# Performance work log

Hardware: AMD Instinct MI355X
Metric: run time of the kernel (lower is better)

The kernel has to match this reference:

```python
import jax, jax.numpy as jnp
import numpy as np

NUM_HEADS = 4

def setup_inputs() -> dict:
    key = jax.random.key(0)
    ks = jax.random.split(key, 8)
    B, L, D, Lc = 4, 4096, 256, 4096
    s = 0.02
    return {
        "x": jax.random.normal(ks[0], (B, L, D), jnp.float32),
        "context": jax.random.normal(ks[1], (B, Lc, D), jnp.float32),
        "Wq": jax.random.normal(ks[2], (D, D), jnp.float32) * s,
        "bq": jax.random.normal(ks[3], (D,), jnp.float32) * s,
        "Wkv": jax.random.normal(ks[4], (D, 2 * D), jnp.float32) * s,
        "bkv": jax.random.normal(ks[5], (2 * D,), jnp.float32) * s,
        "Wp": jax.random.normal(ks[6], (D, D), jnp.float32) * s,
        "bp": jax.random.normal(ks[7], (D,), jnp.float32) * s,
    }


def reference(x, context, Wq, bq, Wkv, bkv, Wp, bp):
    B, L, D = x.shape
    Hn = NUM_HEADS
    hd = D // Hn
    Hs = Ws = int(L ** 0.5)
    scale = hd ** (-0.5)

    # projections
    q = (x @ Wq + bq).reshape(B, L, Hn, hd).transpose(0, 2, 1, 3)        # [B,H,L,hd]
    kv = (context @ Wkv + bkv).reshape(B, -1, 2, Hn, hd)
    k = kv[:, :, 0].transpose(0, 2, 1, 3)                                 # [B,H,Lc,hd]
    v = kv[:, :, 1].transpose(0, 2, 1, 3)                                 # [B,H,Lc,hd]

    attn = jnp.einsum('bhqd,bhkd->bhqk', q, k) * scale                    # [B,H,L,Lc]
    attn_weights = jax.nn.softmax(attn, axis=-1)

    attn_map = attn_weights.mean(axis=1).sum(axis=-1).reshape(B, Hs, Ws)  # [B,H,W]

    out = jnp.einsum('bhqk,bhkd->bhqd', attn_weights, v)                  # [B,H,L,hd]
    out = out.transpose(0, 2, 1, 3).reshape(B, L, D)
    out = out @ Wp + bp
    return (out + x, attn_map)
```

## Files before the change

kernel.cpp:

```cpp
#include <hip/hip_runtime.h>
#include <stdint.h>

typedef unsigned short u16;
typedef short s16x8 __attribute__((ext_vector_type(8)));
typedef u16   u16x8 __attribute__((ext_vector_type(8)));
typedef float f32x4 __attribute__((ext_vector_type(4)));
typedef float f32x16 __attribute__((ext_vector_type(16)));

#define QSCALE 0.180336880111169f

__device__ __forceinline__ u16 f2bf(float f) {
  union { float f; uint32_t u; } v; v.f = f;
  uint32_t r = (v.u + 0x7fffu + ((v.u >> 16) & 1u)) >> 16;
  return (u16)r;
}

__device__ __forceinline__ f32x4 mfma16(s16x8 a, s16x8 b, f32x4 c) {
  return __builtin_amdgcn_mfma_f32_16x16x32_bf16(a, b, c, 0, 0, 0);
}
__device__ __forceinline__ f32x16 mfma32(s16x8 a, s16x8 b, f32x16 c) {
  return __builtin_amdgcn_mfma_f32_32x32x16_bf16(a, b, c, 0, 0, 0);
}

__device__ __forceinline__ void gload16(const void* g, void* l) {
  __builtin_amdgcn_global_load_lds(
      (const __attribute__((address_space(1))) void*)g,
      (__attribute__((address_space(3))) void*)l, 16, 0, 0);
}

__device__ __forceinline__ s16x8 ldsr(const u16* base, int row, int colb) {
  return *(const s16x8*)((const char*)base + row * 128 + (colb ^ ((row & 7) << 4)));
}

__device__ __forceinline__ uint32_t cvtpk(float lo, float hi) {
  uint32_t r;
  asm("v_cvt_pk_bf16_f32 %0, %1, %2" : "=v"(r) : "v"(lo), "v"(hi));
  return r;
}
__device__ __forceinline__ void hswap(uint32_t& a, uint32_t& b) {
  asm("v_permlane32_swap_b32 %0, %1" : "+v"(a), "+v"(b));
}
__device__ __forceinline__ float cross_sum(float v) {
  float t = v, u = v;
  asm("v_permlane32_swap_b32 %0, %1" : "+v"(t), "+v"(u));
  return t + u;
}

__global__ void k_convert(const float* __restrict__ x, const float* __restrict__ ctx,
                          const float* __restrict__ wq, const float* __restrict__ wkv,
                          const float* __restrict__ wp,
                          u16* __restrict__ xb, u16* __restrict__ cb,
                          u16* __restrict__ wqT, u16* __restrict__ wkvT,
                          u16* __restrict__ wpT, float* __restrict__ amap) {
  int tid = blockIdx.x * 256 + threadIdx.x;
  if (tid < 2097152) {
    const float* src; u16* dst; int off;
    if (tid < 1048576) { src = x;   dst = xb; off = tid * 4; }
    else               { src = ctx; dst = cb; off = (tid - 1048576) * 4; }
    f32x4 v = *(const f32x4*)(src + off);
    u16* d = dst + off;
    d[0] = f2bf(v.x); d[1] = f2bf(v.y); d[2] = f2bf(v.z); d[3] = f2bf(v.w);
    if (tid < 16384) amap[tid] = 1.0f;
  } else {
    int t4 = (tid - 2097152) * 4;
#pragma unroll
    for (int j = 0; j < 4; j++) {
      int t = t4 + j;
      if (t < 65536) {
        int k = t >> 8, n = t & 255;
        wqT[n * 256 + k] = f2bf(wq[t]);
      } else if (t < 196608) {
        int t2 = t - 65536;
        int k = t2 >> 9, n = t2 & 511;
        wkvT[n * 256 + k] = f2bf(wkv[t2]);
      } else {
        int t2 = t - 196608;
        int k = t2 >> 8, n = t2 & 255;
        wpT[n * 256 + k] = f2bf(wp[t2]);
      }
    }
  }
}

template<int EPI>
__global__ __launch_bounds__(256, 2) void k_gemm(
    const u16* __restrict__ A, const u16* __restrict__ Bt,
    const float* __restrict__ bias, const float* __restrict__ xres,
    u16* __restrict__ o16a, u16* __restrict__ o16b, float* __restrict__ o32) {
  __shared__ u16 Als[2][128 * 64];
  __shared__ u16 Bls[2][64 * 64];
  const int m0 = blockIdx.x * 128;
  const int n0 = blockIdx.y * 64;
  const int tid = threadIdx.x, w = tid >> 6, l = tid & 63;
  const int lr = l & 15, lg = l >> 4;
  const int wm = (w >> 1) * 64, wn = (w & 1) * 32;

  auto stage = [&](int buf, int k0) {
    const char* sa = (const char*)A;
#pragma unroll
    for (int i = 0; i < 4; i++) {
      int dbase = (w * 4 + i) * 1024;
      int d = dbase + l * 16;
      int row = d >> 7, colb = d & 127;
      gload16(sa + (size_t)(m0 + row) * 512 + k0 * 2 + (colb ^ ((row & 7) << 4)),
              (char*)Als[buf] + dbase);
    }
    const char* sb = (const char*)Bt;
#pragma unroll
    for (int i = 0; i < 2; i++) {
      int dbase = (w * 2 + i) * 1024;
      int d = dbase + l * 16;
      int row = d >> 7, colb = d & 127;
      gload16(sb + (size_t)(n0 + row) * 512 + k0 * 2 + (colb ^ ((row & 7) << 4)),
              (char*)Bls[buf] + dbase);
    }
  };

  f32x4 acc[4][2];
#pragma unroll
  for (int i = 0; i < 4; i++)
#pragma unroll
    for (int j = 0; j < 2; j++) acc[i][j] = (f32x4){0.f, 0.f, 0.f, 0.f};

  stage(0, 0);
  __syncthreads();
  int cur = 0;
  for (int ks = 0; ks < 4; ks++) {
    if (ks < 3) stage(cur ^ 1, (ks + 1) * 64);
    s16x8 a[4][2], b[2][2];
#pragma unroll
    for (int mt = 0; mt < 4; mt++)
#pragma unroll
      for (int kf = 0; kf < 2; kf++)
        a[mt][kf] = ldsr(Als[cur], wm + mt * 16 + lr, lg * 16 + kf * 64);
#pragma unroll
    for (int nt = 0; nt < 2; nt++)
#pragma unroll
      for (int kf = 0; kf < 2; kf++)
        b[nt][kf] = ldsr(Bls[cur], wn + nt * 16 + lr, lg * 16 + kf * 64);
#pragma unroll
    for (int mt = 0; mt < 4; mt++)
#pragma unroll
      for (int nt = 0; nt < 2; nt++) {
        acc[mt][nt] = mfma16(a[mt][0], b[nt][0], acc[mt][nt]);
        acc[mt][nt] = mfma16(a[mt][1], b[nt][1], acc[mt][nt]);
      }
    __syncthreads();
    cur ^= 1;
  }

#pragma unroll
  for (int mt = 0; mt < 4; mt++)
#pragma unroll
    for (int nt = 0; nt < 2; nt++)
#pragma unroll
      for (int r = 0; r < 4; r++) {
        int gm = m0 + wm + mt * 16 + lg * 4 + r;
        int gn = n0 + wn + nt * 16 + lr;
        float val = acc[mt][nt][r] + bias[gn];
        if constexpr (EPI == 0) {
          int b_ = gm >> 12, ql = gm & 4095, h = gn >> 6, dd = gn & 63;
          o16a[(((size_t)(b_ * 4 + h) * 4096 + ql) << 6) + dd] = f2bf(val * QSCALE);
        } else if constexpr (EPI == 1) {
          int b_ = gm >> 12, ql = gm & 4095;
          int s = gn >> 8, inner = gn & 255, h = inner >> 6, dd = inner & 63;
          if (s) {
            size_t addr = (((size_t)(b_ * 4 + h) * 64 + (ql >> 6)) * 64 + dd) * 64 + (ql & 63);
            o16b[addr] = f2bf(val);
          } else {
            size_t addr = (((size_t)(b_ * 4 + h) * 4096 + ql) << 6) + dd;
            o16a[addr] = f2bf(val);
          }
        } else {
          size_t idx = (size_t)gm * 256 + gn;
          o32[idx] = val + xres[idx];
        }
      }
}

__global__ __launch_bounds__(256, 2) void k_flash(
    const u16* __restrict__ qb, const u16* __restrict__ kb,
    const u16* __restrict__ vtb, u16* __restrict__ ob) {
  __shared__ u16 kls[3][4096];
  __shared__ u16 vls[3][4096];
  __shared__ float lsum_lds[4][32];
  const int id = blockIdx.y * 32 + blockIdx.x;
  const int sw = (id & 7) * 64 + (id >> 3);
  const int bh = sw >> 5;
  const int q0 = (sw & 31) * 128;
  const int tid = threadIdx.x, w = tid >> 6, l = tid & 63;
  const int lr32 = l & 31, hi = l >> 5;
  const char* kbase  = (const char*)(kb + (size_t)bh * 262144);
  const char* vtbase = (const char*)(vtb + (size_t)bh * 262144);

  s16x8 qf[4];
  {
    const u16* qp = qb + ((size_t)bh * 4096 + q0 + w * 32 + lr32) * 64 + hi * 8;
#pragma unroll
    for (int mm = 0; mm < 4; mm++) qf[mm] = *(const s16x8*)(qp + mm * 16);
  }

  auto stage = [&](int buf, int t) {
    const char* ks = kbase  + (size_t)t * 8192;
    const char* vs = vtbase + (size_t)t * 8192;
#pragma unroll
    for (int i = 0; i < 2; i++) {
      int dbase = (w * 2 + i) * 1024;
      int d = dbase + l * 16;
      int row = d >> 7, colb = d & 127;
      int so = row * 128 + (colb ^ ((row & 7) << 4));
      gload16(ks + so, (char*)kls[buf] + dbase);
      gload16(vs + so, (char*)vls[buf] + dbase);
    }
  };

  f32x16 o0, o1;
  float lsum = 0.f;
#pragma unroll
  for (int r = 0; r < 16; r++) { o0[r] = 0.f; o1[r] = 0.f; }

  auto pv = [&](const f32x16& p, const u16* vc, int bcol0) {
#pragma unroll
    for (int ks2 = 0; ks2 < 2; ks2++) {
      uint32_t A0 = cvtpk(p[8 * ks2 + 0], p[8 * ks2 + 1]);
      uint32_t A1 = cvtpk(p[8 * ks2 + 2], p[8 * ks2 + 3]);
      uint32_t B0 = cvtpk(p[8 * ks2 + 4], p[8 * ks2 + 5]);
      uint32_t B1 = cvtpk(p[8 * ks2 + 6], p[8 * ks2 + 7]);
      hswap(A0, B0);
      hswap(A1, B1);
      union { uint32_t wv[4]; s16x8 h; } pa;
      pa.wv[0] = A0; pa.wv[1] = A1; pa.wv[2] = B0; pa.wv[3] = B1;
      s16x8 v0 = ldsr(vc, lr32,      bcol0 + 32 * ks2 + 16 * hi);
      s16x8 v1 = ldsr(vc, 32 + lr32, bcol0 + 32 * ks2 + 16 * hi);
      __builtin_amdgcn_s_setprio(1);
      o0 = mfma32(pa.h, v0, o0);
      o1 = mfma32(pa.h, v1, o1);
      __builtin_amdgcn_s_setprio(0);
    }
  };

  stage(0, 0);
  stage(1, 1);
  for (int t = 0; t < 64; t++) {
    if (t < 63) asm volatile("s_waitcnt vmcnt(4)" ::: "memory");
    else        asm volatile("s_waitcnt vmcnt(0)" ::: "memory");
    __builtin_amdgcn_s_barrier();
    asm volatile("" ::: "memory");
    if (t < 62) stage((t + 2) % 3, t + 2);
    const u16* kc = kls[t % 3];
    const u16* vc = vls[t % 3];

    f32x16 s0, s1;
#pragma unroll
    for (int r = 0; r < 16; r++) { s0[r] = 0.f; s1[r] = 0.f; }
    __builtin_amdgcn_s_setprio(1);
#pragma unroll
    for (int mm = 0; mm < 4; mm++) {
      s16x8 kf0 = ldsr(kc, lr32,      mm * 32 + 16 * hi);
      s16x8 kf1 = ldsr(kc, 32 + lr32, mm * 32 + 16 * hi);
      s0 = mfma32(kf0, qf[mm], s0);
      s1 = mfma32(kf1, qf[mm], s1);
    }
    __builtin_amdgcn_s_setprio(0);
#pragma unroll
    for (int r = 0; r < 16; r++) {
      s0[r] = __builtin_amdgcn_exp2f(s0[r]);
      s1[r] = __builtin_amdgcn_exp2f(s1[r]);
    }
    float acc = 0.f;
#pragma unroll
    for (int r = 0; r < 16; r++) acc += s0[r] + s1[r];
    lsum += acc;
    pv(s0, vc, 0);
    pv(s1, vc, 64);
  }

  float ltot = cross_sum(lsum);
  lsum_lds[w][lr32] = ltot;
  const int b_ = bh >> 2, h = bh & 3;
  u16* obase = ob + (size_t)b_ * 4096 * 256 + h * 64;
#pragma unroll
  for (int r = 0; r < 16; r++) {
    int crow = (r & 3) + 8 * (r >> 2) + 4 * hi;
    float inv = __builtin_amdgcn_rcpf(lsum_lds[w][crow]);
    size_t qrow = (size_t)(q0 + w * 32 + crow);
    obase[qrow * 256 + lr32]      = f2bf(o0[r] * inv);
    obase[qrow * 256 + 32 + lr32] = f2bf(o1[r] * inv);
  }
}

extern "C" void kernel_launch(void* const* d_in, const int* in_sizes, int n_in,
                              void* d_out, int out_size, void* d_ws, size_t ws_size,
                              hipStream_t stream) {
  const float* x   = (const float*)d_in[0];
  const float* ctx = (const float*)d_in[1];
  const float* Wq  = (const float*)d_in[2];
  const float* bq  = (const float*)d_in[3];
  const float* Wkv = (const float*)d_in[4];
  const float* bkv = (const float*)d_in[5];
  const float* Wp  = (const float*)d_in[6];
  const float* bp  = (const float*)d_in[7];

  char* ws = (char*)d_ws;
  u16* xb    = (u16*)(ws);
  u16* cb    = (u16*)(ws + 8388608);
  u16* wqT   = (u16*)(ws + 16777216);
  u16* wkvT  = (u16*)(ws + 16908288);
  u16* wpT   = (u16*)(ws + 17170432);
  u16* qbuf  = (u16*)(ws + 17301504);
  u16* kbuf  = (u16*)(ws + 25690112);
  u16* vtbuf = (u16*)(ws + 34078720);
  u16* aout  = (u16*)(ws + 42467328);
  float* out  = (float*)d_out;
  float* amap = out + 4194304;

  k_convert<<<8448, 256, 0, stream>>>(x, ctx, Wq, Wkv, Wp, xb, cb, wqT, wkvT, wpT, amap);
  k_gemm<0><<<dim3(128, 4), 256, 0, stream>>>(xb, wqT, bq, nullptr, qbuf, nullptr, nullptr);
  k_gemm<1><<<dim3(128, 8), 256, 0, stream>>>(cb, wkvT, bkv, nullptr, kbuf, vtbuf, nullptr);
  k_flash<<<dim3(32, 16), 256, 0, stream>>>(qbuf, kbuf, vtbuf, aout);
  k_gemm<2><<<dim3(128, 4), 256, 0, stream>>>(aout, wpT, bp, x, nullptr, nullptr, out);
}
```

Measured before the change: 133.9 us.

## Split KV range across warp pairs in flash kernel with 64-row query tiles

The flash-attention kernel now handles 64 query rows per block instead of 128 and launches twice as many blocks. Within a block, two warps share each 32-row query slice and each takes one half of every 64-key tile. The two partial outputs and row sums are then combined through LDS. The K/V staging moves from a triple buffer to a double buffer with a full vmcnt(0) wait, and launch bounds rise to 4 blocks per CU. The goal is more parallelism and occupancy, at the cost of less prefetch depth, twice the total K/V global reads, and an extra reduction step.

```diff
diff --git a/kernel.cpp b/kernel.cpp
--- a/kernel.cpp
+++ b/kernel.cpp
@@ -178,40 +178,46 @@
       }
 }
 
-__global__ __launch_bounds__(256, 2) void k_flash(
+__global__ __launch_bounds__(256, 4) void k_flash(
     const u16* __restrict__ qb, const u16* __restrict__ kb,
     const u16* __restrict__ vtb, u16* __restrict__ ob) {
-  __shared__ u16 kls[3][4096];
-  __shared__ u16 vls[3][4096];
-  __shared__ float lsum_lds[4][32];
+  __shared__ char smem[33024];
+  u16* kls0 = (u16*)(smem);
+  u16* kls1 = (u16*)(smem + 8192);
+  u16* vls0 = (u16*)(smem + 16384);
+  u16* vls1 = (u16*)(smem + 24576);
+  float* comb = (float*)smem;
+  float* lsb  = (float*)(smem + 32768);
   const int id = blockIdx.y * 32 + blockIdx.x;
-  const int sw = (id & 7) * 64 + (id >> 3);
-  const int bh = sw >> 5;
-  const int q0 = (sw & 31) * 128;
+  const int sw = (id & 7) * 128 + (id >> 3);
+  const int bh = sw >> 6;
+  const int q0 = (sw & 63) * 64;
   const int tid = threadIdx.x, w = tid >> 6, l = tid & 63;
   const int lr32 = l & 31, hi = l >> 5;
+  const int qh = w & 1, kvh = w >> 1;
   const char* kbase  = (const char*)(kb + (size_t)bh * 262144);
   const char* vtbase = (const char*)(vtb + (size_t)bh * 262144);
 
   s16x8 qf[4];
   {
-    const u16* qp = qb + ((size_t)bh * 4096 + q0 + w * 32 + lr32) * 64 + hi * 8;
+    const u16* qp = qb + ((size_t)bh * 4096 + q0 + qh * 32 + lr32) * 64 + hi * 8;
 #pragma unroll
     for (int mm = 0; mm < 4; mm++) qf[mm] = *(const s16x8*)(qp + mm * 16);
   }
 
-  auto stage = [&](int buf, int t) {
+  auto stage = [&](u16* kbuf, u16* vbuf, int t) {
     const char* ks = kbase  + (size_t)t * 8192;
     const char* vs = vtbase + (size_t)t * 8192;
+    int dbase = w * 2048 + (l >> 6) * 1024;
 #pragma unroll
     for (int i = 0; i < 2; i++) {
-      int dbase = (w * 2 + i) * 1024;
-      int d = dbase + l * 16;
+      int d = w * 2048 + i * 1024 + l * 16;
       int row = d >> 7, colb = d & 127;
       int so = row * 128 + (colb ^ ((row & 7) << 4));
-      gload16(ks + so, (char*)kls[buf] + dbase);
-      gload16(vs + so, (char*)vls[buf] + dbase);
-    }
+      gload16(ks + so, (char*)kbuf + d);
+      gload16(vs + so, (char*)vbuf + d);
+    }
+    (void)dbase;
   };
 
   f32x16 o0, o1;
@@ -219,19 +225,37 @@
 #pragma unroll
   for (int r = 0; r < 16; r++) { o0[r] = 0.f; o1[r] = 0.f; }
 
-  auto pv = [&](const f32x16& p, const u16* vc, int bcol0) {
+  auto compute = [&](const u16* kc, const u16* vc) {
+    s16x8 kf[4];
+#pragma unroll
+    for (int mm = 0; mm < 4; mm++)
+      kf[mm] = ldsr(kc, kvh * 32 + lr32, mm * 32 + 16 * hi);
+    f32x16 s;
+#pragma unroll
+    for (int r = 0; r < 16; r++) s[r] = 0.f;
+    __builtin_amdgcn_s_setprio(1);
+#pragma unroll
+    for (int mm = 0; mm < 4; mm++) s = mfma32(kf[mm], qf[mm], s);
+    __builtin_amdgcn_s_setprio(0);
+#pragma unroll
+    for (int r = 0; r < 16; r++) s[r] = __builtin_amdgcn_exp2f(s[r]);
+    float acc = 0.f;
+#pragma unroll
+    for (int r = 0; r < 16; r++) acc += s[r];
+    lsum += acc;
 #pragma unroll
     for (int ks2 = 0; ks2 < 2; ks2++) {
-      uint32_t A0 = cvtpk(p[8 * ks2 + 0], p[8 * ks2 + 1]);
-      uint32_t A1 = cvtpk(p[8 * ks2 + 2], p[8 * ks2 + 3]);
-      uint32_t B0 = cvtpk(p[8 * ks2 + 4], p[8 * ks2 + 5]);
-      uint32_t B1 = cvtpk(p[8 * ks2 + 6], p[8 * ks2 + 7]);
+      uint32_t A0 = cvtpk(s[8 * ks2 + 0], s[8 * ks2 + 1]);
+      uint32_t A1 = cvtpk(s[8 * ks2 + 2], s[8 * ks2 + 3]);
+      uint32_t B0 = cvtpk(s[8 * ks2 + 4], s[8 * ks2 + 5]);
+      uint32_t B1 = cvtpk(s[8 * ks2 + 6], s[8 * ks2 + 7]);
       hswap(A0, B0);
       hswap(A1, B1);
       union { uint32_t wv[4]; s16x8 h; } pa;
       pa.wv[0] = A0; pa.wv[1] = A1; pa.wv[2] = B0; pa.wv[3] = B1;
-      s16x8 v0 = ldsr(vc, lr32,      bcol0 + 32 * ks2 + 16 * hi);
-      s16x8 v1 = ldsr(vc, 32 + lr32, bcol0 + 32 * ks2 + 16 * hi);
+      int vcol = kvh * 64 + 32 * ks2 + 16 * hi;
+      s16x8 v0 = ldsr(vc, lr32,      vcol);
+      s16x8 v1 = ldsr(vc, 32 + lr32, vcol);
       __builtin_amdgcn_s_setprio(1);
       o0 = mfma32(pa.h, v0, o0);
       o1 = mfma32(pa.h, v1, o1);
@@ -239,53 +263,47 @@
     }
   };
 
-  stage(0, 0);
-  stage(1, 1);
-  for (int t = 0; t < 64; t++) {
-    if (t < 63) asm volatile("s_waitcnt vmcnt(4)" ::: "memory");
-    else        asm volatile("s_waitcnt vmcnt(0)" ::: "memory");
+  stage(kls0, vls0, 0);
+#pragma unroll 1
+  for (int tt = 0; tt < 32; tt++) {
+    const int t = tt * 2;
+    asm volatile("s_waitcnt vmcnt(0)" ::: "memory");
     __builtin_amdgcn_s_barrier();
     asm volatile("" ::: "memory");
-    if (t < 62) stage((t + 2) % 3, t + 2);
-    const u16* kc = kls[t % 3];
-    const u16* vc = vls[t % 3];
-
-    f32x16 s0, s1;
-#pragma unroll
-    for (int r = 0; r < 16; r++) { s0[r] = 0.f; s1[r] = 0.f; }
-    __builtin_amdgcn_s_setprio(1);
-#pragma unroll
-    for (int mm = 0; mm < 4; mm++) {
-      s16x8 kf0 = ldsr(kc, lr32,      mm * 32 + 16 * hi);
-      s16x8 kf1 = ldsr(kc, 32 + lr32, mm * 32 + 16 * hi);
-      s0 = mfma32(kf0, qf[mm], s0);
-      s1 = mfma32(kf1, qf[mm], s1);
-    }
-    __builtin_amdgcn_s_setprio(0);
+    stage(kls1, vls1, t + 1);
+    compute(kls0, vls0);
+    asm volatile("s_waitcnt vmcnt(0)" ::: "memory");
+    __builtin_amdgcn_s_barrier();
+    asm volatile("" ::: "memory");
+    if (t + 2 < 64) stage(kls0, vls0, t + 2);
+    compute(kls1, vls1);
+  }
+
+  float ltot = cross_sum(lsum);
+  __syncthreads();
+  if (kvh == 1) {
+    float* cp = comb + ((size_t)qh * 64 + l) * 33;
+#pragma unroll
+    for (int r = 0; r < 16; r++) { cp[r] = o0[r]; cp[16 + r] = o1[r]; }
+    cp[32] = ltot;
+  }
+  __syncthreads();
+  if (kvh == 0) {
+    const float* cp = comb + ((size_t)qh * 64 + l) * 33;
+#pragma unroll
+    for (int r = 0; r < 16; r++) { o0[r] += cp[r]; o1[r] += cp[16 + r]; }
+    ltot += cp[32];
+    lsb[qh * 32 + lr32] = ltot;
+    const int b_ = bh >> 2, h = bh & 3;
+    u16* obase = ob + (size_t)b_ * 4096 * 256 + h * 64;
 #pragma unroll
     for (int r = 0; r < 16; r++) {
-      s0[r] = __builtin_amdgcn_exp2f(s0[r]);
-      s1[r] = __builtin_amdgcn_exp2f(s1[r]);
-    }
-    float acc = 0.f;
-#pragma unroll
-    for (int r = 0; r < 16; r++) acc += s0[r] + s1[r];
-    lsum += acc;
-    pv(s0, vc, 0);
-    pv(s1, vc, 64);
-  }
-
-  float ltot = cross_sum(lsum);
-  lsum_lds[w][lr32] = ltot;
-  const int b_ = bh >> 2, h = bh & 3;
-  u16* obase = ob + (size_t)b_ * 4096 * 256 + h * 64;
-#pragma unroll
-  for (int r = 0; r < 16; r++) {
-    int crow = (r & 3) + 8 * (r >> 2) + 4 * hi;
-    float inv = __builtin_amdgcn_rcpf(lsum_lds[w][crow]);
-    size_t qrow = (size_t)(q0 + w * 32 + crow);
-    obase[qrow * 256 + lr32]      = f2bf(o0[r] * inv);
-    obase[qrow * 256 + 32 + lr32] = f2bf(o1[r] * inv);
+      int crow = (r & 3) + 8 * (r >> 2) + 4 * hi;
+      float inv = __builtin_amdgcn_rcpf(lsb[qh * 32 + crow]);
+      size_t qrow = (size_t)(q0 + qh * 32 + crow);
+      obase[qrow * 256 + lr32]      = f2bf(o0[r] * inv);
+      obase[qrow * 256 + 32 + lr32] = f2bf(o1[r] * inv);
+    }
   }
 }
 
@@ -317,6 +335,6 @@
   k_convert<<<8448, 256, 0, stream>>>(x, ctx, Wq, Wkv, Wp, xb, cb, wqT, wkvT, wpT, amap);
   k_gemm<0><<<dim3(128, 4), 256, 0, stream>>>(xb, wqT, bq, nullptr, qbuf, nullptr, nullptr);
   k_gemm<1><<<dim3(128, 8), 256, 0, stream>>>(cb, wkvT, bkv, nullptr, kbuf, vtbuf, nullptr);
-  k_flash<<<dim3(32, 16), 256, 0, stream>>>(qbuf, kbuf, vtbuf, aout);
+  k_flash<<<dim3(32, 32), 256, 0, stream>>>(qbuf, kbuf, vtbuf, aout);
   k_gemm<2><<<dim3(128, 4), 256, 0, stream>>>(aout, wpT, bp, x, nullptr, nullptr, out);
 }
```

New measurement: 136.9 us. 1.02x slower.
